# Optimization experiments

Hardware: AMD Instinct MI355X
Metric: run time of the kernel (lower is better)

The kernel has to match this reference:

```python
import jax, jax.numpy as jnp
import numpy as np

B, C, N, H = 2, 512, 2048, 8
DK = C // H  # 64


def entmax15(z):
    """Exact 1.5-entmax over last axis (Peters & Martins 2019, sort-based)."""
    z = z / 2.0
    z = z - jnp.max(z, axis=-1, keepdims=True)
    zs = -jnp.sort(-z, axis=-1)  # descending sort
    n = zs.shape[-1]
    rho = jnp.arange(1, n + 1, dtype=z.dtype)
    mean = jnp.cumsum(zs, axis=-1) / rho
    mean_sq = jnp.cumsum(zs * zs, axis=-1) / rho
    ss = rho * (mean_sq - mean * mean)
    delta = (1.0 - ss) / rho
    tau = mean - jnp.sqrt(jnp.clip(delta, 1e-12))
    support = jnp.sum((tau <= zs).astype(jnp.int32), axis=-1)
    tau_star = jnp.take_along_axis(tau, (support - 1)[..., None], axis=-1)
    return jnp.square(jnp.clip(z - tau_star, 0.0))


def layernorm(x, a, b, eps=1e-6):
    # matches the custom LayerNorm: unbiased std (torch default), eps added to std
    mean = jnp.mean(x, axis=-1, keepdims=True)
    std = jnp.sqrt(jnp.var(x, axis=-1, ddof=1, keepdims=True))
    return a * (x - mean) / (std + eps) + b


def setup_inputs() -> dict:
    key = jax.random.key(0)
    ks = jax.random.split(key, 7)
    s = 1.0 / np.sqrt(C)  # torch Linear init range
    u = lambda k, shp: jax.random.uniform(k, shp, jnp.float32, -s, s)
    return {
        "x": jax.random.normal(ks[0], (B, C, N), jnp.float32),
        "Wq": u(ks[1], (C, C)), "bq": u(ks[2], (C,)),
        "Wk": u(ks[3], (C, C)), "bk": u(ks[4], (C,)),
        "Wv": u(ks[5], (C, C)), "bv": u(ks[6], (C,)),
        "a2": jnp.ones((C,), jnp.float32),
        "b2": jnp.ones((C,), jnp.float32),
    }


def reference(x, Wq, bq, Wk, bk, Wv, bv, a2, b2):
    xt = jnp.transpose(x, (0, 2, 1))  # (B, N, C)
    x_res = xt

    def heads(W, bias):
        y = xt @ W.T + bias  # torch Linear: x @ W.T + b
        return jnp.transpose(y.reshape(B, N, H, DK), (0, 2, 1, 3))  # (B,H,N,DK)

    q, k, v = heads(Wq, bq), heads(Wk, bk), heads(Wv, bv)
    energy = jnp.einsum("bhqd,bhkd->bhqk", q, k) / np.sqrt(DK)
    p = entmax15(energy)  # sparse attention weights
    o = jnp.einsum("bhqk,bhkd->bhqd", p, v)
    o = jnp.transpose(o, (0, 2, 1, 3)).reshape(B, N, C)
    # dropouts are identity in eval mode
    return x_res + layernorm(o, a2, b2)
```

## Files before the change

### kernel.cpp

```cpp
#include <hip/hip_runtime.h>

typedef _Float16 f16;
typedef _Float16 f16x2 __attribute__((ext_vector_type(2)));
typedef _Float16 f16x4 __attribute__((ext_vector_type(4)));
typedef _Float16 f16x8 __attribute__((ext_vector_type(8)));
typedef float    f32x4 __attribute__((ext_vector_type(4)));

#define B_  2
#define C_  512
#define N_  2048
#define H_  8
#define DK_ 64
#define BH_ 16
#define NIT 8

static __device__ __forceinline__ f16x2 cvt_pk(float a, float b) {
  return __builtin_bit_cast(f16x2, __builtin_amdgcn_cvt_pkrtz(a, b));
}

#if defined(__has_builtin)
#if __has_builtin(__builtin_amdgcn_fdot2)
#define FDOT2(a,b,c) __builtin_amdgcn_fdot2((a),(b),(c),false)
#endif
#endif
#ifndef FDOT2
static __device__ __forceinline__ float FDOT2(f16x2 a, f16x2 b, float c) {
  return c + (float)a[0]*(float)b[0] + (float)a[1]*(float)b[1];
}
#endif

#define MFMA16(a,b,acc) __builtin_amdgcn_mfma_f32_16x16x32_f16((a),(b),(acc),0,0,0)


__global__ __launch_bounds__(256) void prep_x(const float* __restrict__ x,
                                              f16* __restrict__ xT)
{
  const int nt = blockIdx.x, mt = blockIdx.y, b = blockIdx.z;
  const int n0 = nt * 64, m0 = mt * 64;
  __shared__ float tile[64][65];
  const int t = threadIdx.x;
  {
    const int ml = t >> 2, nc = (t & 3) * 16;
    const float* src = x + ((size_t)(b * C_ + m0 + ml)) * N_ + n0 + nc;
    *(float4*)&tile[ml][nc]      = *(const float4*)(src);
    *(float4*)&tile[ml][nc + 4]  = *(const float4*)(src + 4);
    *(float4*)&tile[ml][nc + 8]  = *(const float4*)(src + 8);
    *(float4*)&tile[ml][nc + 12] = *(const float4*)(src + 12);
  }
  __syncthreads();
  {
    const int nl = t >> 2, mc = (t & 3) * 16;
    f16x8 o0, o1;
    #pragma unroll
    for (int i = 0; i < 8; ++i) {
      o0[i] = (f16)tile[mc + i][nl];
      o1[i] = (f16)tile[mc + 8 + i][nl];
    }
    f16* dst = xT + ((size_t)(b * N_ + n0 + nl)) * C_ + m0 + mc;
    *(f16x8*)(dst)     = o0;
    *(f16x8*)(dst + 8) = o1;
  }
}

__global__ __launch_bounds__(256) void qkv_lds(
    const f16* __restrict__ xT,
    const float* __restrict__ Wq, const float* __restrict__ Wk,
    const float* __restrict__ Wv,
    const float* __restrict__ bq, const float* __restrict__ bk,
    const float* __restrict__ bv,
    f16* __restrict__ q16, f16* __restrict__ k16, f16* __restrict__ vT16)
{
  const int nt = blockIdx.x, ctb = blockIdx.y, z = blockIdx.z;
  const int b = z / 3, mat = z % 3;
  const float* W    = (mat == 0) ? Wq : (mat == 1) ? Wk : Wv;
  const float* bias = (mat == 0) ? bq : (mat == 1) ? bk : bv;
  const int n0 = nt * 128, c0 = ctb * 64;

  __shared__ f16 As[128 * 64];
  __shared__ f16 Bs[64 * 64];

  const int t = threadIdx.x, w = t >> 6, lane = t & 63;
  const int c = lane & 15, g = lane >> 4;

  const int rB0 = t >> 3, dS = t & 7;
  const int rB1 = rB0 + 32;
  const f16* aSrc[4];
  #pragma unroll
  for (int u = 0; u < 4; ++u) {
    const int r = rB0 + 32 * u;
    aSrc[u] = xT + (size_t)(b * N_ + n0 + r) * C_ + 8 * (dS ^ (r & 7));
  }
  const float* wSrc0 = W + (size_t)(c0 + rB0) * C_ + 8 * (dS ^ (rB0 & 7));
  const float* wSrc1 = W + (size_t)(c0 + rB1) * C_ + 8 * (dS ^ (rB1 & 7));

  f32x4 acc[2][4] = {};
  #pragma unroll 1
  for (int k0 = 0; k0 < C_; k0 += 64) {
    #pragma unroll
    for (int u = 0; u < 4; ++u)
      *(f16x8*)&As[(rB0 + 32 * u) * 64 + 8 * dS] = *(const f16x8*)(aSrc[u] + k0);
    {
      float4 u0 = *(const float4*)(wSrc0 + k0);
      float4 u1 = *(const float4*)(wSrc0 + k0 + 4);
      union { f16x8 v8; f16x2 v2[4]; } u;
      u.v2[0] = cvt_pk(u0.x, u0.y); u.v2[1] = cvt_pk(u0.z, u0.w);
      u.v2[2] = cvt_pk(u1.x, u1.y); u.v2[3] = cvt_pk(u1.z, u1.w);
      *(f16x8*)&Bs[rB0 * 64 + 8 * dS] = u.v8;
    }
    {
      float4 u0 = *(const float4*)(wSrc1 + k0);
      float4 u1 = *(const float4*)(wSrc1 + k0 + 4);
      union { f16x8 v8; f16x2 v2[4]; } u;
      u.v2[0] = cvt_pk(u0.x, u0.y); u.v2[1] = cvt_pk(u0.z, u0.w);
      u.v2[2] = cvt_pk(u1.x, u1.y); u.v2[3] = cvt_pk(u1.z, u1.w);
      *(f16x8*)&Bs[rB1 * 64 + 8 * dS] = u.v8;
    }
    __syncthreads();
    const int ar0 = 32 * w + c, ar1 = ar0 + 16;
    f16x8 a00 = *(const f16x8*)&As[ar0 * 64 + 8 * (g ^ (ar0 & 7))];
    f16x8 a01 = *(const f16x8*)&As[ar0 * 64 + 8 * ((4 + g) ^ (ar0 & 7))];
    f16x8 a10 = *(const f16x8*)&As[ar1 * 64 + 8 * (g ^ (ar1 & 7))];
    f16x8 a11 = *(const f16x8*)&As[ar1 * 64 + 8 * ((4 + g) ^ (ar1 & 7))];
    #pragma unroll
    for (int ct = 0; ct < 4; ++ct) {
      const int br = ct * 16 + c;
      f16x8 b0 = *(const f16x8*)&Bs[br * 64 + 8 * (g ^ (br & 7))];
      f16x8 b1 = *(const f16x8*)&Bs[br * 64 + 8 * ((4 + g) ^ (br & 7))];
      acc[0][ct] = MFMA16(a00, b0, acc[0][ct]);
      acc[0][ct] = MFMA16(a01, b1, acc[0][ct]);
      acc[1][ct] = MFMA16(a10, b0, acc[1][ct]);
      acc[1][ct] = MFMA16(a11, b1, acc[1][ct]);
    }
    __syncthreads();
  }

  #pragma unroll
  for (int rf = 0; rf < 2; ++rf) {
    #pragma unroll
    for (int ct = 0; ct < 4; ++ct) {
      const int ccol = c0 + ct * 16 + c;
      const float bb = bias[ccol];
      const int h2 = ccol >> 6;
      const int bh = b * H_ + h2;
      if (mat == 2) {
        const int dih = ccol & 63, dt = dih >> 4, cp = dih & 15;
        const int jc = (n0 + 32 * w) >> 5;
        f16* vp = vT16 + (((size_t)(bh * 4 + dt)) * 64 + jc) * 512
                       + 128 * g + 8 * cp + rf;
        #pragma unroll
        for (int e = 0; e < 4; ++e)
          vp[2 * e] = (f16)(acc[rf][ct][e] + bb);
      } else {
        const int d = ccol & 63, kk = d >> 5, gp = (d >> 3) & 3, ii = d & 7;
        const int jt = (n0 + 32 * w + 16 * rf) >> 4;
        f16* out = (mat == 0) ? q16 : k16;
        const float sc = (mat == 0) ? 0.0625f : 1.0f;
        f16* op = out + (((size_t)(bh * 128 + jt)) * 2 + kk) * 512
                      + 128 * gp + 32 * g + ii;
        #pragma unroll
        for (int e = 0; e < 4; ++e)
          op[8 * e] = (f16)((acc[rf][ct][e] + bb) * sc);
      }
    }
  }
}

__global__ __launch_bounds__(256, 4) void attn(
    const f16* __restrict__ q16, const f16* __restrict__ k16,
    const f16* __restrict__ vT16, float* __restrict__ o)
{
  const int id = blockIdx.x;
  const int bh = id & 15;
  const int n0 = (id >> 4) * 16;
  const int t = threadIdx.x;
  const int w = t >> 6, lane = t & 63;
  const int c = lane & 15, g = lane >> 4;

  __shared__ f16 p_lds[16 * 520];
  __shared__ float red[2][4][16][2];

  const f16* Qb = q16  + (size_t)bh * (128 * 2 * 512);
  const f16* Kb = k16  + (size_t)bh * (128 * 2 * 512);
  const f16* Vb = vT16 + (size_t)bh * (4 * 64 * 512);

  const f16* qp = Qb + (size_t)(n0 >> 4) * 1024 + 8 * lane;
  f16x8 qa0 = *(const f16x8*)(qp);
  f16x8 qa1 = *(const f16x8*)(qp + 512);

  f16x2 z2[64];
  #pragma unroll
  for (int tt = 0; tt < 16; ++tt) {
    const f16* kp = Kb + (size_t)(32 * w + 2 * tt) * 1024 + 8 * lane;
    f16x8 kb00 = *(const f16x8*)(kp);
    f16x8 kb01 = *(const f16x8*)(kp + 512);
    f16x8 kb10 = *(const f16x8*)(kp + 1024);
    f16x8 kb11 = *(const f16x8*)(kp + 1536);
    f32x4 a0 = {}, a1 = {};
    a0 = MFMA16(qa0, kb00, a0);
    a0 = MFMA16(qa1, kb01, a0);
    a1 = MFMA16(qa0, kb10, a1);
    a1 = MFMA16(qa1, kb11, a1);
    #pragma unroll
    for (int e = 0; e < 4; ++e)
      z2[tt * 4 + e] = cvt_pk(a0[e], a1[e]);
  }

  f16x2 m2[4];
  #pragma unroll
  for (int e = 0; e < 4; ++e) m2[e] = z2[e];
  #pragma unroll
  for (int tt = 1; tt < 16; ++tt)
    #pragma unroll
    for (int e = 0; e < 4; ++e)
      m2[e] = __builtin_elementwise_max(m2[e], z2[tt * 4 + e]);
  float m[4];
  #pragma unroll
  for (int e = 0; e < 4; ++e) m[e] = fmaxf((float)m2[e][0], (float)m2[e][1]);
  #pragma unroll
  for (int dm = 1; dm <= 8; dm <<= 1)
    #pragma unroll
    for (int e = 0; e < 4; ++e) m[e] = fmaxf(m[e], __shfl_xor(m[e], dm, 64));
  if (c == 0) {
    #pragma unroll
    for (int e = 0; e < 4; ++e) red[0][w][4 * g + e][0] = m[e];
  }
  __syncthreads();
  #pragma unroll
  for (int e = 0; e < 4; ++e) {
    const int r = 4 * g + e;
    m[e] = fmaxf(fmaxf(red[0][0][r][0], red[0][1][r][0]),
                 fmaxf(red[0][2][r][0], red[0][3][r][0]));
  }

  float tau[4];
  #pragma unroll
  for (int e = 0; e < 4; ++e) tau[e] = m[e] - 1.f;

  const f16x2 one2  = {(_Float16)1.f, (_Float16)1.f};
  const f16x2 zero2 = {(_Float16)0.f, (_Float16)0.f};

  #pragma unroll 1
  for (int it = 0; it < NIT; ++it) {
    const int pb = (it + 1) & 1;
    f16x2 tau2[4];
    #pragma unroll
    for (int e = 0; e < 4; ++e)
      tau2[e] = cvt_pk(tau[e], tau[e]);
    float S1[4] = {0.f, 0.f, 0.f, 0.f}, S2[4] = {0.f, 0.f, 0.f, 0.f};
    #pragma unroll
    for (int tt = 0; tt < 16; ++tt)
      #pragma unroll
      for (int e = 0; e < 4; ++e) {
        f16x2 d2 = z2[tt * 4 + e] - tau2[e];
        d2 = __builtin_elementwise_max(d2, zero2);
        S1[e] = FDOT2(d2, one2, S1[e]);
        S2[e] = FDOT2(d2, d2, S2[e]);
      }
    #pragma unroll
    for (int dm = 1; dm <= 8; dm <<= 1)
      #pragma unroll
      for (int e = 0; e < 4; ++e) {
        S1[e] += __shfl_xor(S1[e], dm, 64);
        S2[e] += __shfl_xor(S2[e], dm, 64);
      }
    if (c == 0) {
      #pragma unroll
      for (int e = 0; e < 4; ++e) {
        red[pb][w][4 * g + e][0] = S1[e];
        red[pb][w][4 * g + e][1] = S2[e];
      }
    }
    __syncthreads();
    #pragma unroll
    for (int e = 0; e < 4; ++e) {
      const int r = 4 * g + e;
      float s1 = red[pb][0][r][0] + red[pb][1][r][0] + red[pb][2][r][0] + red[pb][3][r][0];
      float s2 = red[pb][0][r][1] + red[pb][1][r][1] + red[pb][2][r][1] + red[pb][3][r][1];
      tau[e] = fminf(tau[e] + (s2 - 1.f) / (2.f * s1 + 1e-20f), m[e] - 0.01f);
    }
  }

  {
    f16x2 tau2[4];
    #pragma unroll
    for (int e = 0; e < 4; ++e)
      tau2[e] = cvt_pk(tau[e], tau[e]);
    #pragma unroll
    for (int tt = 0; tt < 16; ++tt)
      #pragma unroll
      for (int e = 0; e < 4; ++e) {
        f16x2 d2 = z2[tt * 4 + e] - tau2[e];
        d2 = __builtin_elementwise_max(d2, zero2);
        z2[tt * 4 + e] = d2 * d2;
      }
  }

  f32x4 oacc = {};
  #pragma unroll 1
  for (int q = 0; q < 4; ++q) {
    if (w == q) {
      #pragma unroll
      for (int tt = 0; tt < 16; ++tt)
        #pragma unroll
        for (int e = 0; e < 4; ++e) {
          const int row = 4 * g + e;
          *(f16x2*)&p_lds[row * 520 + 32 * tt + 2 * c] = z2[tt * 4 + e];
        }
    }
    __syncthreads();
    #pragma unroll
    for (int T = 0; T < 16; ++T) {
      f16x8 pa = *(f16x8*)&p_lds[c * 520 + 32 * T + 8 * g];
      f16x8 vb = *(const f16x8*)(Vb + ((size_t)w * 64 + 16 * q + T) * 512 + 8 * lane);
      oacc = MFMA16(pa, vb, oacc);
    }
    __syncthreads();
  }

  const int b = bh >> 3, h = bh & 7;
  #pragma unroll
  for (int e = 0; e < 4; ++e)
    o[((size_t)b * N_ + n0 + 4 * g + e) * C_ + h * 64 + 16 * w + c] = oacc[e];
}

__global__ __launch_bounds__(256) void ln_res(
    const float* __restrict__ o, const float* __restrict__ x,
    const float* __restrict__ a2, const float* __restrict__ b2,
    float* __restrict__ out)
{
  const int row0 = blockIdx.x * 8;
  const int b = row0 >> 11, nl = row0 & (N_ - 1);
  const int t = threadIdx.x;
  __shared__ float xres[8][516];
  {
    #pragma unroll
    for (int rep = 0; rep < 2; ++rep) {
      const int cc = t + rep * 256;
      const float* xp = x + ((size_t)(b * C_ + cc)) * N_ + nl;
      float4 u0 = *(const float4*)(xp);
      float4 u1 = *(const float4*)(xp + 4);
      xres[0][cc] = u0.x; xres[1][cc] = u0.y; xres[2][cc] = u0.z; xres[3][cc] = u0.w;
      xres[4][cc] = u1.x; xres[5][cc] = u1.y; xres[6][cc] = u1.z; xres[7][cc] = u1.w;
    }
  }
  __syncthreads();
  const int w = t >> 6, lane = t & 63;
  #pragma unroll
  for (int rr = 0; rr < 2; ++rr) {
    const int r = w * 2 + rr;
    const size_t row = (size_t)row0 + r;
    float v[8];
    #pragma unroll
    for (int i = 0; i < 8; ++i) v[i] = o[row * C_ + lane + 64 * i];
    float s = 0.f, ss = 0.f;
    #pragma unroll
    for (int i = 0; i < 8; ++i) { s += v[i]; ss = fmaf(v[i], v[i], ss); }
    #pragma unroll
    for (int dm = 1; dm <= 32; dm <<= 1) {
      s  += __shfl_xor(s, dm, 64);
      ss += __shfl_xor(ss, dm, 64);
    }
    const float mean = s * (1.f / C_);
    float var = (ss - (float)C_ * mean * mean) * (1.f / (C_ - 1));
    var = fmaxf(var, 0.f);
    const float rd = 1.f / (sqrtf(var) + 1e-6f);
    #pragma unroll
    for (int i = 0; i < 8; ++i) {
      const int cc = lane + 64 * i;
      out[row * C_ + cc] = a2[cc] * (v[i] - mean) * rd + b2[cc] + xres[r][cc];
    }
  }
}

extern "C" void kernel_launch(void* const* d_in, const int* in_sizes, int n_in,
                              void* d_out, int out_size, void* d_ws, size_t ws_size,
                              hipStream_t stream)
{
  const float* x  = (const float*)d_in[0];
  const float* Wq = (const float*)d_in[1];
  const float* bq = (const float*)d_in[2];
  const float* Wk = (const float*)d_in[3];
  const float* bk = (const float*)d_in[4];
  const float* Wv = (const float*)d_in[5];
  const float* bv = (const float*)d_in[6];
  const float* a2 = (const float*)d_in[7];
  const float* b2 = (const float*)d_in[8];

  const size_t HEADSZ = (size_t)BH_ * N_ * DK_;
  f16* q16  = (f16*)d_ws;
  f16* k16  = q16 + HEADSZ;
  f16* vT16 = k16 + HEADSZ;

  f16* xT16 = (f16*)d_out;
  float* o  = (float*)d_out;

  prep_x <<<dim3(32, 8, 2),  256, 0, stream>>>(x, xT16);
  qkv_lds<<<dim3(16, 8, 6),  256, 0, stream>>>(xT16, Wq, Wk, Wv, bq, bk, bv,
                                               q16, k16, vT16);
  attn   <<<dim3(2048),      256, 0, stream>>>(q16, k16, vT16, o);
  ln_res <<<dim3(512),       256, 0, stream>>>(o, x, a2, b2, (float*)d_out);
}
```

Before: 186.2 us.

## Pre-convert weights to fp16 and double-buffer QKV GEMM with direct global-to-LDS loads

Adds a small kernel that converts Wq/Wk/Wv to fp16 once per call into spare output space, so the QKV GEMM no longer reloads and converts fp32 weights in every tile. The GEMM now double-buffers its LDS tiles and, when the builtin is available, uses global_load_lds to stage A and B straight into shared memory, overlapping the next tile's loads with the current MFMA work. This costs an extra kernel launch, extra weight traffic, and twice the LDS, which may reduce occupancy. The QKV projection is likely a small share of total time, since the attention kernel probably dominates.

```diff
diff --git a/kernel.cpp b/kernel.cpp
--- a/kernel.cpp
+++ b/kernel.cpp
@@ -21,6 +21,9 @@
 #if defined(__has_builtin)
 #if __has_builtin(__builtin_amdgcn_fdot2)
 #define FDOT2(a,b,c) __builtin_amdgcn_fdot2((a),(b),(c),false)
+#endif
+#if __has_builtin(__builtin_amdgcn_global_load_lds)
+#define HAS_GLL 1
 #endif
 #endif
 #ifndef FDOT2
@@ -62,77 +65,107 @@
   }
 }
 
-__global__ __launch_bounds__(256) void qkv_lds(
-    const f16* __restrict__ xT,
+__global__ __launch_bounds__(256) void wconv(
     const float* __restrict__ Wq, const float* __restrict__ Wk,
-    const float* __restrict__ Wv,
+    const float* __restrict__ Wv, f16* __restrict__ W16)
+{
+  const int mat = blockIdx.y;
+  const float* W = (mat == 0) ? Wq : (mat == 1) ? Wk : Wv;
+  const int idx = (blockIdx.x * 256 + threadIdx.x) * 8;
+  float4 u0 = *(const float4*)(W + idx);
+  float4 u1 = *(const float4*)(W + idx + 4);
+  union { f16x8 v8; f16x2 v2[4]; } u;
+  u.v2[0] = cvt_pk(u0.x, u0.y); u.v2[1] = cvt_pk(u0.z, u0.w);
+  u.v2[2] = cvt_pk(u1.x, u1.y); u.v2[3] = cvt_pk(u1.z, u1.w);
+  *(f16x8*)(W16 + (size_t)mat * C_ * C_ + idx) = u.v8;
+}
+
+__global__ __launch_bounds__(256) void qkv_gl(
+    const f16* __restrict__ xT, const f16* __restrict__ W16,
     const float* __restrict__ bq, const float* __restrict__ bk,
     const float* __restrict__ bv,
     f16* __restrict__ q16, f16* __restrict__ k16, f16* __restrict__ vT16)
 {
   const int nt = blockIdx.x, ctb = blockIdx.y, z = blockIdx.z;
   const int b = z / 3, mat = z % 3;
-  const float* W    = (mat == 0) ? Wq : (mat == 1) ? Wk : Wv;
   const float* bias = (mat == 0) ? bq : (mat == 1) ? bk : bv;
+  const f16* Wm = W16 + (size_t)mat * C_ * C_;
   const int n0 = nt * 128, c0 = ctb * 64;
 
-  __shared__ f16 As[128 * 64];
-  __shared__ f16 Bs[64 * 64];
+  __shared__ f16 As[2][128 * 64];
+  __shared__ f16 Bs[2][64 * 64];
 
   const int t = threadIdx.x, w = t >> 6, lane = t & 63;
   const int c = lane & 15, g = lane >> 4;
 
-  const int rB0 = t >> 3, dS = t & 7;
-  const int rB1 = rB0 + 32;
-  const f16* aSrc[4];
+  const int li = lane >> 3, dS = lane & 7;
+  const f16* aS[4];
   #pragma unroll
   for (int u = 0; u < 4; ++u) {
-    const int r = rB0 + 32 * u;
-    aSrc[u] = xT + (size_t)(b * N_ + n0 + r) * C_ + 8 * (dS ^ (r & 7));
-  }
-  const float* wSrc0 = W + (size_t)(c0 + rB0) * C_ + 8 * (dS ^ (rB0 & 7));
-  const float* wSrc1 = W + (size_t)(c0 + rB1) * C_ + 8 * (dS ^ (rB1 & 7));
+    const int r = 32 * w + 8 * u + li;
+    aS[u] = xT + (size_t)(b * N_ + n0 + r) * C_ + 8 * (dS ^ (r & 7));
+  }
+  const f16* bS[2];
+  #pragma unroll
+  for (int u = 0; u < 2; ++u) {
+    const int r = 16 * w + 8 * u + li;
+    bS[u] = Wm + (size_t)(c0 + r) * C_ + 8 * (dS ^ (r & 7));
+  }
+
+#ifdef HAS_GLL
+#define STAGE(buf, k0)                                                          \
+  do {                                                                          \
+    _Pragma("unroll")                                                           \
+    for (int u = 0; u < 4; ++u)                                                 \
+      __builtin_amdgcn_global_load_lds(                                         \
+          (const __attribute__((address_space(1))) void*)(aS[u] + (k0)),        \
+          (__attribute__((address_space(3))) void*)(&As[buf][512 * (4 * w + u)]),\
+          16, 0, 0);                                                            \
+    _Pragma("unroll")                                                           \
+    for (int u = 0; u < 2; ++u)                                                 \
+      __builtin_amdgcn_global_load_lds(                                         \
+          (const __attribute__((address_space(1))) void*)(bS[u] + (k0)),        \
+          (__attribute__((address_space(3))) void*)(&Bs[buf][512 * (2 * w + u)]),\
+          16, 0, 0);                                                            \
+  } while (0)
+#else
+#define STAGE(buf, k0)                                                          \
+  do {                                                                          \
+    _Pragma("unroll")                                                           \
+    for (int u = 0; u < 4; ++u)                                                 \
+      *(f16x8*)&As[buf][512 * (4 * w + u) + 8 * lane] = *(const f16x8*)(aS[u] + (k0)); \
+    _Pragma("unroll")                                                           \
+    for (int u = 0; u < 2; ++u)                                                 \
+      *(f16x8*)&Bs[buf][512 * (2 * w + u) + 8 * lane] = *(const f16x8*)(bS[u] + (k0)); \
+  } while (0)
+#endif
 
   f32x4 acc[2][4] = {};
+  STAGE(0, 0);
+  __syncthreads();
+  int cur = 0;
   #pragma unroll 1
-  for (int k0 = 0; k0 < C_; k0 += 64) {
-    #pragma unroll
-    for (int u = 0; u < 4; ++u)
-      *(f16x8*)&As[(rB0 + 32 * u) * 64 + 8 * dS] = *(const f16x8*)(aSrc[u] + k0);
-    {
-      float4 u0 = *(const float4*)(wSrc0 + k0);
-      float4 u1 = *(const float4*)(wSrc0 + k0 + 4);
-      union { f16x8 v8; f16x2 v2[4]; } u;
-      u.v2[0] = cvt_pk(u0.x, u0.y); u.v2[1] = cvt_pk(u0.z, u0.w);
-      u.v2[2] = cvt_pk(u1.x, u1.y); u.v2[3] = cvt_pk(u1.z, u1.w);
-      *(f16x8*)&Bs[rB0 * 64 + 8 * dS] = u.v8;
-    }
-    {
-      float4 u0 = *(const float4*)(wSrc1 + k0);
-      float4 u1 = *(const float4*)(wSrc1 + k0 + 4);
-      union { f16x8 v8; f16x2 v2[4]; } u;
-      u.v2[0] = cvt_pk(u0.x, u0.y); u.v2[1] = cvt_pk(u0.z, u0.w);
-      u.v2[2] = cvt_pk(u1.x, u1.y); u.v2[3] = cvt_pk(u1.z, u1.w);
-      *(f16x8*)&Bs[rB1 * 64 + 8 * dS] = u.v8;
-    }
-    __syncthreads();
+  for (int ks = 0; ks < 8; ++ks) {
+    if (ks < 7) STAGE(cur ^ 1, 64 * (ks + 1));
     const int ar0 = 32 * w + c, ar1 = ar0 + 16;
-    f16x8 a00 = *(const f16x8*)&As[ar0 * 64 + 8 * (g ^ (ar0 & 7))];
-    f16x8 a01 = *(const f16x8*)&As[ar0 * 64 + 8 * ((4 + g) ^ (ar0 & 7))];
-    f16x8 a10 = *(const f16x8*)&As[ar1 * 64 + 8 * (g ^ (ar1 & 7))];
-    f16x8 a11 = *(const f16x8*)&As[ar1 * 64 + 8 * ((4 + g) ^ (ar1 & 7))];
+    f16x8 a00 = *(const f16x8*)&As[cur][ar0 * 64 + 8 * (g ^ (ar0 & 7))];
+    f16x8 a01 = *(const f16x8*)&As[cur][ar0 * 64 + 8 * ((4 + g) ^ (ar0 & 7))];
+    f16x8 a10 = *(const f16x8*)&As[cur][ar1 * 64 + 8 * (g ^ (ar1 & 7))];
+    f16x8 a11 = *(const f16x8*)&As[cur][ar1 * 64 + 8 * ((4 + g) ^ (ar1 & 7))];
     #pragma unroll
     for (int ct = 0; ct < 4; ++ct) {
       const int br = ct * 16 + c;
-      f16x8 b0 = *(const f16x8*)&Bs[br * 64 + 8 * (g ^ (br & 7))];
-      f16x8 b1 = *(const f16x8*)&Bs[br * 64 + 8 * ((4 + g) ^ (br & 7))];
+      f16x8 b0 = *(const f16x8*)&Bs[cur][br * 64 + 8 * (g ^ (br & 7))];
+      f16x8 b1 = *(const f16x8*)&Bs[cur][br * 64 + 8 * ((4 + g) ^ (br & 7))];
       acc[0][ct] = MFMA16(a00, b0, acc[0][ct]);
       acc[0][ct] = MFMA16(a01, b1, acc[0][ct]);
       acc[1][ct] = MFMA16(a10, b0, acc[1][ct]);
       acc[1][ct] = MFMA16(a11, b1, acc[1][ct]);
     }
     __syncthreads();
-  }
+    cur ^= 1;
+  }
+#undef STAGE
 
   #pragma unroll
   for (int rf = 0; rf < 2; ++rf) {
@@ -392,10 +425,12 @@
   f16* vT16 = k16 + HEADSZ;
 
   f16* xT16 = (f16*)d_out;
+  f16* W16  = xT16 + (size_t)B_ * N_ * C_;
   float* o  = (float*)d_out;
 
   prep_x <<<dim3(32, 8, 2),  256, 0, stream>>>(x, xT16);
-  qkv_lds<<<dim3(16, 8, 6),  256, 0, stream>>>(xT16, Wq, Wk, Wv, bq, bk, bv,
+  wconv  <<<dim3(128, 3),    256, 0, stream>>>(Wq, Wk, Wv, W16);
+  qkv_gl <<<dim3(16, 8, 6),  256, 0, stream>>>(xT16, W16, bq, bk, bv,
                                                q16, k16, vT16);
   attn   <<<dim3(2048),      256, 0, stream>>>(q16, k16, vT16, o);
   ln_res <<<dim3(512),       256, 0, stream>>>(o, x, a2, b2, (float*)d_out);
```

Result: no change. 189.2 us (+1.6%).
